# Kernel tuning notes

Hardware: AMD Instinct MI355X
Metric: run time of the kernel (lower is better)

Reference implementation:

```python
import jax, jax.numpy as jnp
import numpy as np

CLP_K = 9
SCL_KS = (3, 4, 3)  # scl0_k, scl1_k, scl2_k from the source


def _ste(f, x):
    # straight-through estimator: forward f(x), identity gradient
    return x + jax.lax.stop_gradient(f(x) - x)


def floor_ste(x):
    return _ste(jnp.floor, x)


def round_ste(x):
    return _ste(jnp.round, x)


def conv_t(x, w, b):
    # torch F.conv_transpose2d with kernel 5, stride 2, padding 2, output_padding 1
    # expressed as an lhs-dilated conv; w is torch layout [in, out, kh, kw]
    k = w.shape[-1]
    wc = jnp.flip(w, axis=(-2, -1)).transpose(1, 0, 2, 3)  # -> [out, in, kh, kw]
    lo = k - 1 - 2           # k-1-padding = 2
    hi = k - 1 - 2 + 1       # + output_padding = 3
    y = jax.lax.conv_general_dilated(
        x, wc, window_strides=(1, 1), padding=[(lo, hi), (lo, hi)],
        lhs_dilation=(2, 2), dimension_numbers=('NCHW', 'OIHW', 'NCHW'))
    return y + b[None, :, None, None]


def split_deconv(x, w, b, split):
    # sum of `split` transposed convs with floor((round(W)+j)/split) quantized weights
    out = 0.0
    for j in range(split):
        wj = floor_ste((round_ste(w) + j) / split)
        bj = floor_ste((round_ste(b) + j) / split)
        out = out + conv_t(x, wj, bj)
    return out


def _g_s_forward(x, ws, bs, ms, relus, dv, Bits, split):
    # clp[i] = round((2^Bits - 1) / relus[i] * 2^(16+clp_k))
    clp = jnp.round((2.0 ** Bits - 1.0) / relus * 2.0 ** (16 + CLP_K))
    for i in range(3):
        x = split_deconv(x, ws[i], bs[i], split)
        x = x * ms[i][None, :, None, None]
        x = floor_ste((x + 2.0 ** (dv[i] - 1 - CLP_K)) / 2.0 ** (dv[i] - CLP_K))
        x = jnp.clip(x, 0.0, clp[i])
        sk = SCL_KS[i]
        scl = floor_ste((relus[i] + 2.0 ** (sk - 1)) / 2.0 ** sk)
        x = floor_ste((x * scl + 2.0 ** (15 + CLP_K - sk)) / 2.0 ** (16 + CLP_K - sk))
    x = split_deconv(x, ws[3], bs[3], split)
    x = x * ms[3][None, :, None, None]
    x = floor_ste((x + 2.0 ** (dv[3] - 9)) / 2.0 ** (dv[3] - 8))
    return x / 255.0


def setup_inputs() -> dict:
    key = jax.random.key(0)
    ks = jax.random.split(key, 16)
    N, M = 192, 320
    B, h, w = 1, 48, 48
    x = jax.random.randint(ks[0], (B, M, h, w), 0, 256).astype(jnp.float32)
    w1 = jax.random.normal(ks[1], (M, N, 5, 5), jnp.float32) * 20.0
    b1 = jax.random.normal(ks[2], (N,), jnp.float32) * 20.0
    w2 = jax.random.normal(ks[3], (N, N, 5, 5), jnp.float32) * 20.0
    b2 = jax.random.normal(ks[4], (N,), jnp.float32) * 20.0
    w3 = jax.random.normal(ks[5], (N, N, 5, 5), jnp.float32) * 20.0
    b3 = jax.random.normal(ks[6], (N,), jnp.float32) * 20.0
    w4 = jax.random.normal(ks[7], (N, 3, 5, 5), jnp.float32) * 20.0
    b4 = jax.random.normal(ks[8], (3,), jnp.float32) * 20.0
    muls0 = jax.random.randint(ks[9], (N,), 1, 1000).astype(jnp.float32)
    muls1 = jax.random.randint(ks[10], (N,), 1, 1000).astype(jnp.float32)
    muls2 = jax.random.randint(ks[11], (N,), 1, 1000).astype(jnp.float32)
    muls3 = jax.random.randint(ks[12], (3,), 1, 1000).astype(jnp.float32)
    relus = jnp.array([40000.0, 36000.0, 30000.0], jnp.float32)
    muls_dvds = jnp.array([24, 24, 24, 24], jnp.int32)
    return {"x": x, "w1": w1, "b1": b1, "w2": w2, "b2": b2, "w3": w3,
            "b3": b3, "w4": w4, "b4": b4, "muls0": muls0, "muls1": muls1,
            "muls2": muls2, "muls3": muls3, "relus": relus,
            "muls_dvds": muls_dvds, "Bits": 8, "split": 4}


def reference(x, w1, b1, w2, b2, w3, b3, w4, b4,
              muls0, muls1, muls2, muls3, relus, muls_dvds, Bits, split):
    dv = muls_dvds.astype(jnp.float32)
    ws = (w1, w2, w3, w4)
    bs = (b1, b2, b3, b4)
    ms = (muls0, muls1, muls2, muls3)
    return _g_s_forward(x, ws, bs, ms, relus, dv, int(Bits), int(split))
```

## Files before the change

### kernel.cpp

```cpp
#include <hip/hip_runtime.h>
#include <cmath>


typedef int int4v  __attribute__((ext_vector_type(4)));
typedef int int16v __attribute__((ext_vector_type(16)));

#define GLOBAL_AS __attribute__((address_space(1)))
#define LDS_AS    __attribute__((address_space(3)))

__device__ __forceinline__ void dma16(const signed char* g, signed char* l) {
    __builtin_amdgcn_global_load_lds((const GLOBAL_AS int*)g, (LDS_AS int*)l,
                                     16, 0, 0);
}

__device__ __forceinline__ void tap_to_k(int t, int& ky, int& kx) {
    if (t < 9)       { int dy = t/3,  dx = t%3;                   ky = 4-2*dy; kx = 4-2*dx; }
    else if (t < 15) { int u = t-9;   int dy = u/2, dx = 1+(u&1);  ky = 4-2*dy; kx = 5-2*dx; }
    else if (t < 21) { int u = t-15;  int dy = 1+u/3, dx = u%3;    ky = 5-2*dy; kx = 4-2*dx; }
    else             { int u = t-21;  int dy = 1+u/2, dx = 1+(u&1); ky = 5-2*dy; kx = 5-2*dx; }
}

__global__ __launch_bounds__(256)
void convert_x_t(const float* __restrict__ x, signed char* __restrict__ xh,
                 int* __restrict__ tsz, int ts_count, int C, int HW,
                 signed char* __restrict__ xpad) {
    if (blockIdx.x == 0 && blockIdx.y == 0) {
        for (int i = threadIdx.x; i < ts_count; i += 256) tsz[i] = 0;
        if (threadIdx.x < 128) ((int*)xpad)[threadIdx.x] = (int)0x80808080;
    }
    __shared__ float t[64][65];
    const int p0 = blockIdx.x * 64;
    const int c0 = blockIdx.y * 64;
    const int pL = threadIdx.x & 63;
    const int r0 = threadIdx.x >> 6;
    #pragma unroll
    for (int k = 0; k < 16; ++k) {
        int ciL = r0 * 16 + k;
        t[ciL][pL] = x[(size_t)(c0 + ciL) * HW + p0 + pL];
    }
    __syncthreads();
    #pragma unroll
    for (int k = 0; k < 16; ++k) {
        int pL2 = r0 * 16 + k;
        xh[(size_t)(p0 + pL2) * C + c0 + pL] = (signed char)((int)t[pL][pL2] - 128);
    }
}

__global__ __launch_bounds__(256)
void prep_pack(const float* __restrict__ w1, const float* __restrict__ w2,
               const float* __restrict__ w3, const float* __restrict__ w4,
               signed char* __restrict__ p1, signed char* __restrict__ p2,
               signed char* __restrict__ p3, signed char* __restrict__ p4,
               int* __restrict__ t1, int* __restrict__ t2, int* __restrict__ t3,
               int* __restrict__ t4) {
    const int layer = blockIdx.y;
    if (layer == 3) {
        const int bx = blockIdx.x;
        if (bx < 54) {
            #pragma unroll
            for (int k = 0; k < 4; ++k) {
                int idx = bx * 1024 + k * 256 + threadIdx.x;
                int j    = idx & 15;
                int lane = (idx >> 4) & 63;
                int rem  = idx >> 10;
                int s9   = rem % 9;
                int qs   = rem / 9;
                int col  = lane & 31;
                int co   = col & 7;
                int p    = col >> 3;
                int py = p >> 1, px = p & 1;
                int dy = s9 / 3, dx = s9 % 3;
                int ci = qs * 32 + ((lane >> 5) << 4) + j;
                bool part = (py == 0 || dy >= 1) && (px == 0 || dx >= 1);
                float v = 0.0f;
                if (co < 3 && part) {
                    int ky = py ? 5 - 2 * dy : 4 - 2 * dy;
                    int kx = px ? 5 - 2 * dx : 4 - 2 * dx;
                    v = rintf(w4[(size_t)(ci * 3 + co) * 25 + ky * 5 + kx]);
                    v = fminf(fmaxf(v, -128.0f), 127.0f);
                }
                p4[idx] = (signed char)(int)v;
            }
        } else if (threadIdx.x < 128) {
            const int Cin = 192, Cout = 3;
            const int u = (bx - 54) * 2 + (threadIdx.x >> 6);
            const int lane = threadIdx.x & 63;
            const int co = u % Cout, p = u / Cout;
            const int py = p >> 1, px = p & 1;
            const int nky = (5 - py + 1) >> 1;
            const int nkx = (5 - px + 1) >> 1;
            const int ntap = nky * nkx;
            int s = 0;
            for (int idx = lane; idx < Cin * ntap; idx += 64) {
                const int ci = idx / ntap;
                const int uu = idx - ci * ntap;
                const int ky = py + 2 * (uu / nkx);
                const int kx = px + 2 * (uu % nkx);
                float v = rintf(w4[(size_t)(ci * Cout + co) * 25 + ky * 5 + kx]);
                v = fminf(fmaxf(v, -128.0f), 127.0f);
                s += (int)v;
            }
            #pragma unroll
            for (int off = 32; off > 0; off >>= 1)
                s += __shfl_down(s, off, 64);
            if (lane == 0) t4[u] = s;
        }
        return;
    }
    const float* w = (layer == 0) ? w1 : (layer == 1) ? w2 : w3;
    signed char* out = (layer == 0) ? p1 : (layer == 1) ? p2 : p3;
    int* ts = (layer == 0) ? t1 : (layer == 1) ? t2 : t3;
    const int Cout = 192;
    const int s = blockIdx.x;
    if (layer > 0 && s >= 36) return;
    const int qs = s / 6, nb = s % 6;

    __shared__ __align__(16) signed char ls[25600];
    __shared__ int lsum[4][32];
    if (threadIdx.x < 128) ((int*)lsum)[threadIdx.x] = 0;
    __syncthreads();

    #pragma unroll
    for (int k = 0; k < 4; ++k) {
        const int pidx = threadIdx.x + k * 256;
        const int cil = pidx >> 5;
        const int col = pidx & 31;
        const int ci = qs * 32 + cil;
        const int co = nb * 32 + col;
        const float* wr = w + (size_t)(ci * Cout + co) * 25;
        const int half = cil >> 4, j = cil & 15;
        const int base = (half * 32 + col) * 16 + j;
        int psum[4] = {0, 0, 0, 0};
        #pragma unroll
        for (int t = 0; t < 25; ++t) {
            int ky, kx; tap_to_k(t, ky, kx);
            float v = rintf(wr[ky * 5 + kx]);
            v = fminf(fmaxf(v, -128.0f), 127.0f);
            int iv = (int)v;
            ls[t * 1024 + base] = (signed char)iv;
            psum[((ky & 1) << 1) | (kx & 1)] += iv;
        }
        #pragma unroll
        for (int p = 0; p < 4; ++p) atomicAdd(&lsum[p][col], psum[p]);
    }
    __syncthreads();

    signed char* dst = out + (size_t)s * 25600;
    for (int i = threadIdx.x; i < 1600; i += 256)
        *(int4v*)&dst[i * 16] = *(const int4v*)&ls[i * 16];
    if (threadIdx.x < 128) {
        const int p = threadIdx.x >> 5, col = threadIdx.x & 31;
        atomicAdd(&ts[p * Cout + nb * 32 + col], lsum[p][col]);
    }
}

__device__ __forceinline__ constexpr int role_nt(int role, int s9) {
    constexpr int NT0[9] = {1,1,1,1,2,2,1,2,2};
    constexpr int NT1[9] = {0,1,1,1,2,2,1,2,2};
    return role == 0 ? NT0[s9] : NT1[s9];
}
__device__ __forceinline__ constexpr int role_tap(int role, int s9, int u) {
    constexpr int T0[9][2] = {{0,0},{1,0},{2,0},{3,0},{4,21},{5,22},{6,0},{7,23},{8,24}};
    constexpr int T1[9][2] = {{0,0},{9,0},{10,0},{15,0},{11,16},{12,17},{18,0},{13,19},{14,20}};
    return role == 0 ? T0[s9][u] : T1[s9][u];
}
__device__ __forceinline__ constexpr int role_acc(int role, int s9, int u) {
    constexpr int A0[9][2] = {{0,0},{0,0},{0,0},{0,0},{0,1},{0,1},{0,0},{0,1},{0,1}};
    constexpr int A1[9][2] = {{0,0},{0,0},{0,0},{1,0},{0,1},{0,1},{1,0},{0,1},{0,1}};
    return role == 0 ? A0[s9][u] : A1[s9][u];
}

template<int ROLE, int R>
__device__ __forceinline__ void compute_role(const signed char* xsb, const signed char* bsb,
                                             int16v (&acc)[R][2], const int (&p0)[R],
                                             int half, int lane) {
    #pragma unroll
    for (int s9 = 0; s9 < 9; ++s9) {
        if (role_nt(ROLE, s9) == 0) continue;
        const int dy = s9 / 3, dx = s9 % 3;
        int4v a[R];
        #pragma unroll
        for (int r = 0; r < R; ++r)
            a[r] = *(const int4v*)&xsb[(p0[r] + dy * 18 + dx) * 32 + half * 16];
        #pragma unroll
        for (int u = 0; u < 2; ++u) {
            if (u < role_nt(ROLE, s9)) {
                int4v b = *(const int4v*)&bsb[role_tap(ROLE, s9, u) * 1024 + lane * 16];
                const int ai = role_acc(ROLE, s9, u);
                #pragma unroll
                for (int r = 0; r < R; ++r)
                    acc[r][ai] = __builtin_amdgcn_mfma_i32_32x32x32_i8(a[r], b, acc[r][ai], 0, 0, 0);
            }
        }
    }
}

template<int MW, int R, bool BDBUF>
__global__ __launch_bounds__(MW * 64, 4)
void deconv_v14(const signed char* __restrict__ xin, const signed char* __restrict__ wpk,
                const float* __restrict__ bias, const float* __restrict__ muls,
                const int* __restrict__ tsum,
                const float* __restrict__ relus, const int* __restrict__ dvds,
                const int* __restrict__ bitsp, const signed char* __restrict__ xpad,
                int layer, int Cin, int Cout, int NT, int Hq, int Wq,
                int NB, int NQX, int T8,
                signed char* __restrict__ outp) {
    constexpr int PAIRS = MW / 2;
    constexpr int QROWS = PAIRS * R * 2;
    constexpr int NROW = QROWS + 2;
    constexpr int NPIX = NROW * 18;
    constexpr int THREADS = MW * 64;
    constexpr int XC = NPIX * 2;
    constexpr int XI = (XC + THREADS - 1) / THREADS;
    constexpr int BC = 1600;
    constexpr int BI = (BC + THREADS - 1) / THREADS;
    constexpr int NBS = BDBUF ? 2 : 1;

    __shared__ __align__(16) signed char xs[2][NPIX * 32];
    __shared__ __align__(16) signed char bs[NBS][25600];

    const int tid  = threadIdx.x;
    const int lane = tid & 63;
    const int wid  = tid >> 6;
    const int pairId = wid >> 1;
    const int role   = wid & 1;

    int nb, qx, qy;
    {
        const int bi = blockIdx.x;
        if (T8 > 0) {
            const int xcd = bi & 7, j = bi >> 3;
            const int tl = j / NB, n = j - tl * NB;
            const int tile = xcd * T8 + tl;
            nb = n; qx = tile % NQX; qy = tile / NQX;
        } else {
            nb = bi % NB;
            const int s = bi / NB;
            qx = s % NQX; qy = s / NQX;
        }
    }
    const int qx0 = qx * 16;
    const int qy0 = qy * QROWS;
    const int n0  = nb * 32;

    int16v acc[R][2];
    #pragma unroll
    for (int r = 0; r < R; ++r)
        #pragma unroll
        for (int p = 0; p < 2; ++p)
            #pragma unroll
            for (int e = 0; e < 16; ++e) acc[r][p][e] = 0;

    const int half   = lane >> 5;
    const int rowbit = (lane >> 4) & 1;
    const int col    = lane & 15;
    int p0[R];
    #pragma unroll
    for (int r = 0; r < R; ++r)
        p0[r] = ((pairId * R + r) * 2 + rowbit) * 18 + col;

    const signed char* xsrc[XI];
    #pragma unroll
    for (int t = 0; t < XI; ++t) {
        int i = tid + t * THREADS;
        xsrc[t] = xpad;
        if (i < XC) {
            int pix = i >> 1, g = i & 1;
            int rr = pix / 18, cc = pix - rr * 18;
            int y = qy0 - 1 + rr, xx = qx0 - 1 + cc;
            bool ok = (unsigned)y < (unsigned)Hq && (unsigned)xx < (unsigned)Wq;
            xsrc[t] = ok ? (xin + ((size_t)y * Wq + xx) * Cin + g * 16)
                         : (xpad + g * 16);
        }
    }

    auto dma_x = [&](int ck, int b) {
        #pragma unroll
        for (int t = 0; t < XI; ++t) {
            int i = tid + t * THREADS;
            if (i < XC) dma16(xsrc[t] + ck, &xs[b][i * 16]);
        }
    };
    auto dma_b = [&](int cs, int b) {
        const signed char* ws = wpk + (size_t)(cs * NT + nb) * 25600;
        #pragma unroll
        for (int t = 0; t < BI; ++t) {
            int i = tid + t * THREADS;
            if (i < BC) dma16(ws + (size_t)i * 16, &bs[b][i * 16]);
        }
    };

    dma_x(0, 0);
    if (BDBUF) dma_b(0, 0);
    for (int ck = 0, s = 0; ck < Cin; ck += 32, ++s) {
        const int cb = s & 1;
        if (BDBUF) {
            __syncthreads();
            if (ck + 32 < Cin) {
                dma_x(s + 1, cb ^ 1) , dma_b(s + 1, cb ^ 1);
            }
            if (role == 0) compute_role<0, R>(xs[cb], bs[cb], acc, p0, half, lane);
            else           compute_role<1, R>(xs[cb], bs[cb], acc, p0, half, lane);
        } else {
            __syncthreads();
            dma_b(s, 0);
            if (ck + 32 < Cin) dma_x(s + 1, cb ^ 1);
            __syncthreads();
            if (role == 0) compute_role<0, R>(xs[cb], bs[0], acc, p0, half, lane);
            else           compute_role<1, R>(xs[cb], bs[0], acc, p0, half, lane);
        }
    }

    const int dv = dvds[layer];
    float add1 = ldexpf(1.0f, dv - 10);
    float inv1 = ldexpf(1.0f, -(dv - 9));
    const float relu = relus[layer];
    const int sk = (layer == 1) ? 4 : 3;
    const float bitsv = ldexpf(1.0f, bitsp[0]) - 1.0f;
    float clp, scl;
    {
        #pragma clang fp contract(off)
        clp = rintf(bitsv / relu * 33554432.0f);
        scl = floorf((relu + ldexpf(1.0f, sk - 1)) * ldexpf(1.0f, -sk));
    }
    float add2 = ldexpf(1.0f, 24 - sk);
    float inv2 = ldexpf(1.0f, -(25 - sk));

    const int co = n0 + (lane & 31);
    float bq = rintf(bias[co]);
    float mm = muls[co];
    int pmap[2];
    pmap[0] = role == 0 ? 0 : 1;
    pmap[1] = role == 0 ? 3 : 2;
    int fullp[2];
    #pragma unroll
    for (int a = 0; a < 2; ++a) fullp[a] = tsum[pmap[a] * Cout + co];

    const int Wout = Wq * 2;

    #pragma unroll
    for (int r = 0; r < R; ++r) {
        #pragma unroll
        for (int a = 0; a < 2; ++a) {
            const int p = pmap[a];
            const int py = p >> 1, px = p & 1;
            #pragma unroll
            for (int reg = 0; reg < 16; ++reg) {
                const int mrow = (reg & 3) + 8 * (reg >> 2) + 4 * (lane >> 5);
                const int qy2 = qy0 + (pairId * R + r) * 2 + (mrow >> 4);
                const int qx2 = qx0 + (mrow & 15);
                float v = (float)(acc[r][a][reg] + 128 * fullp[a]);
                {
                    #pragma clang fp contract(off)
                    v = (v + bq) * mm;
                    v = floorf((v + add1) * inv1);
                    v = fminf(fmaxf(v, 0.0f), clp);
                    v = floorf((v * scl + add2) * inv2);
                }
                const int oy = 2 * qy2 + py, ox = 2 * qx2 + px;
                outp[((size_t)oy * Wout + ox) * Cout + co] = (signed char)((int)v - 128);
            }
        }
    }
}

__global__ __launch_bounds__(256, 4)
void deconv_final_v14(const signed char* __restrict__ xin, const signed char* __restrict__ wpk,
                      const float* __restrict__ bias, const float* __restrict__ muls,
                      const int* __restrict__ tsum, const int* __restrict__ dvds,
                      const signed char* __restrict__ xpad,
                      int Cin, int Hq, int Wq, float* __restrict__ outp) {
    constexpr int R = 2, MW = 4;
    constexpr int QROWS = MW * R * 2;
    constexpr int NROW = QROWS + 2;
    constexpr int NPIX = NROW * 18;
    constexpr int THREADS = 256;
    constexpr int XC = NPIX * 2;
    constexpr int XI = (XC + THREADS - 1) / THREADS;
    constexpr int BC = 576;
    constexpr int BI = (BC + THREADS - 1) / THREADS;

    __shared__ __align__(16) signed char xs[2][NPIX * 32];
    __shared__ __align__(16) signed char bs[2][9216];

    const int tid  = threadIdx.x;
    const int lane = tid & 63;
    const int wid  = tid >> 6;
    const int qx0  = blockIdx.y * 16;
    const int qy0  = blockIdx.z * QROWS;

    int16v acc[R];
    #pragma unroll
    for (int r = 0; r < R; ++r)
        #pragma unroll
        for (int e = 0; e < 16; ++e) acc[r][e] = 0;

    const int half   = lane >> 5;
    const int rowbit = (lane >> 4) & 1;
    const int col    = lane & 15;
    int p0[R];
    #pragma unroll
    for (int r = 0; r < R; ++r)
        p0[r] = ((wid * R + r) * 2 + rowbit) * 18 + col;

    const signed char* xsrc[XI];
    #pragma unroll
    for (int t = 0; t < XI; ++t) {
        int i = tid + t * THREADS;
        xsrc[t] = xpad;
        if (i < XC) {
            int pix = i >> 1, g = i & 1;
            int rr = pix / 18, cc = pix - rr * 18;
            int y = qy0 - 1 + rr, xx = qx0 - 1 + cc;
            bool ok = (unsigned)y < (unsigned)Hq && (unsigned)xx < (unsigned)Wq;
            xsrc[t] = ok ? (xin + ((size_t)y * Wq + xx) * Cin + g * 16)
                         : (xpad + g * 16);
        }
    }

    auto dma_x = [&](int ck, int b) {
        #pragma unroll
        for (int t = 0; t < XI; ++t) {
            int i = tid + t * THREADS;
            if (i < XC) dma16(xsrc[t] + ck, &xs[b][i * 16]);
        }
    };
    auto dma_b = [&](int cs, int b) {
        const signed char* ws = wpk + (size_t)cs * 9216;
        #pragma unroll
        for (int t = 0; t < BI; ++t) {
            int i = tid + t * THREADS;
            if (i < BC) dma16(ws + (size_t)i * 16, &bs[b][i * 16]);
        }
    };

    dma_x(0, 0);
    dma_b(0, 0);
    for (int ck = 0; ck < Cin; ck += 32) {
        const int cb = (ck >> 5) & 1;
        __syncthreads();
        if (ck + 32 < Cin) {
            dma_x(ck + 32, cb ^ 1);
            dma_b((ck >> 5) + 1, cb ^ 1);
        }
        #pragma unroll
        for (int s9 = 0; s9 < 9; ++s9) {
            const int dy = s9 / 3, dx = s9 % 3;
            int4v b = *(const int4v*)&bs[cb][s9 * 1024 + lane * 16];
            #pragma unroll
            for (int r = 0; r < R; ++r) {
                int4v a = *(const int4v*)&xs[cb][(p0[r] + dy * 18 + dx) * 32 + half * 16];
                acc[r] = __builtin_amdgcn_mfma_i32_32x32x32_i8(a, b, acc[r], 0, 0, 0);
            }
        }
    }

    const int dv = dvds[3];
    const float add1 = ldexpf(1.0f, dv - 9);
    const float inv1 = ldexpf(1.0f, -(dv - 8));

    const int coln = lane & 31;
    const int co = coln & 7;
    const int p  = coln >> 3;
    const int py = p >> 1, px = p & 1;
    const bool valid = (co < 3);
    float bq = 0.f, mm = 0.f;
    int fp = 0;
    if (valid) { bq = rintf(bias[co]); mm = muls[co]; fp = tsum[p * 3 + co]; }

    const int Wout = Wq * 2, Hout = Hq * 2;
    #pragma unroll
    for (int r = 0; r < R; ++r) {
        #pragma unroll
        for (int reg = 0; reg < 16; ++reg) {
            const int mrow = (reg & 3) + 8 * (reg >> 2) + 4 * (lane >> 5);
            const int qy = qy0 + (wid * R + r) * 2 + (mrow >> 4);
            const int qx = qx0 + (mrow & 15);
            float v = (float)(acc[r][reg] + 128 * fp);
            {
                #pragma clang fp contract(off)
                v = (v + bq) * mm;
                v = floorf((v + add1) * inv1);
                v = v / 255.0f;
            }
            if (valid) {
                const int oy = 2 * qy + py, ox = 2 * qx + px;
                outp[((size_t)co * Hout + oy) * Wout + ox] = v;
            }
        }
    }
}

extern "C" void kernel_launch(void* const* d_in, const int* in_sizes, int n_in,
                              void* d_out, int out_size, void* d_ws, size_t ws_size,
                              hipStream_t stream) {
    const float* x  = (const float*)d_in[0];
    const float* w1 = (const float*)d_in[1];
    const float* b1 = (const float*)d_in[2];
    const float* w2 = (const float*)d_in[3];
    const float* b2 = (const float*)d_in[4];
    const float* w3 = (const float*)d_in[5];
    const float* b3 = (const float*)d_in[6];
    const float* w4 = (const float*)d_in[7];
    const float* b4 = (const float*)d_in[8];
    const float* m0 = (const float*)d_in[9];
    const float* m1 = (const float*)d_in[10];
    const float* m2 = (const float*)d_in[11];
    const float* m3 = (const float*)d_in[12];
    const float* relus = (const float*)d_in[13];
    const int* dvds = (const int*)d_in[14];
    const int* bitsp = (const int*)d_in[15];

    signed char* wsb = (signed char*)d_ws;
    size_t o = 0;
    signed char* wpk1 = wsb + o; o += (size_t)10 * 6 * 25600;
    signed char* wpk2 = wsb + o; o += (size_t)6 * 6 * 25600;
    signed char* wpk3 = wsb + o; o += (size_t)6 * 6 * 25600;
    signed char* wpk4 = wsb + o; o += (size_t)6 * 9216;
    int* ts1 = (int*)(wsb + o); o += 4 * 192 * 4;
    int* ts2 = (int*)(wsb + o); o += 4 * 192 * 4;
    int* ts3 = (int*)(wsb + o); o += 4 * 192 * 4;
    int* ts4 = (int*)(wsb + o); o += 4 * 4 * 4;
    o = (o + 15) & ~(size_t)15;
    signed char* xpad = wsb + o; o += 512;
    signed char* xh = wsb + o; o += (size_t)48 * 48 * 320;
    signed char* a1 = wsb + o; o += (size_t)96 * 96 * 192;
    signed char* a2 = wsb + o; o += (size_t)192 * 192 * 192;
    signed char* a3 = wsb + o; o += (size_t)384 * 384 * 192;

    const int ts_count = 4 * 192 * 3 + 4 * 4;

    convert_x_t<<<dim3(36, 5), 256, 0, stream>>>(x, xh, ts1, ts_count, 320, 48 * 48, xpad);
    prep_pack<<<dim3(60, 4), 256, 0, stream>>>(w1, w2, w3, w4,
                                               wpk1, wpk2, wpk3, wpk4,
                                               ts1, ts2, ts3, ts4);

    deconv_v14<4, 2, true><<<108, 256, 0, stream>>>(
        xh, wpk1, b1, m0, ts1, relus, dvds, bitsp, xpad, 0, 320, 192, 6, 48, 48,
        6, 3, 0, a1);
    deconv_v14<4, 2, false><<<432, 256, 0, stream>>>(
        a1, wpk2, b2, m1, ts2, relus, dvds, bitsp, xpad, 1, 192, 192, 6, 96, 96,
        6, 6, 0, a2);
    deconv_v14<4, 2, false><<<1728, 256, 0, stream>>>(
        a2, wpk3, b3, m2, ts3, relus, dvds, bitsp, xpad, 2, 192, 192, 6, 192, 192,
        6, 12, 36, a3);
    deconv_final_v14<<<dim3(1, 24, 24), 256, 0, stream>>>(
        a3, wpk4, b4, m3, ts4, dvds, xpad, 192, 384, 384, (float*)d_out);
}
```

Before: 202.9 us.

## Fuse prep, layer-1 and layer-2 deconvs into one persistent kernel with grid barriers

```diff
diff --git a/kernel.cpp b/kernel.cpp
--- a/kernel.cpp
+++ b/kernel.cpp
@@ -11,6 +11,18 @@
 __device__ __forceinline__ void dma16(const signed char* g, signed char* l) {
     __builtin_amdgcn_global_load_lds((const GLOBAL_AS int*)g, (LDS_AS int*)l,
                                      16, 0, 0);
+}
+
+__device__ __forceinline__ void gbar(int* bar, int phase, int nblk) {
+    __threadfence();
+    __syncthreads();
+    if (threadIdx.x == 0) {
+        __hip_atomic_fetch_add(bar, 1, __ATOMIC_RELEASE, __HIP_MEMORY_SCOPE_AGENT);
+        const int tgt = phase * nblk;
+        while (__hip_atomic_load(bar, __ATOMIC_ACQUIRE, __HIP_MEMORY_SCOPE_AGENT) < tgt)
+            __builtin_amdgcn_s_sleep(8);
+    }
+    __syncthreads();
 }
 
 __device__ __forceinline__ void tap_to_k(int t, int& ky, int& kx) {
@@ -18,140 +30,6 @@
     else if (t < 15) { int u = t-9;   int dy = u/2, dx = 1+(u&1);  ky = 4-2*dy; kx = 5-2*dx; }
     else if (t < 21) { int u = t-15;  int dy = 1+u/3, dx = u%3;    ky = 5-2*dy; kx = 4-2*dx; }
     else             { int u = t-21;  int dy = 1+u/2, dx = 1+(u&1); ky = 5-2*dy; kx = 5-2*dx; }
-}
-
-__global__ __launch_bounds__(256)
-void convert_x_t(const float* __restrict__ x, signed char* __restrict__ xh,
-                 int* __restrict__ tsz, int ts_count, int C, int HW,
-                 signed char* __restrict__ xpad) {
-    if (blockIdx.x == 0 && blockIdx.y == 0) {
-        for (int i = threadIdx.x; i < ts_count; i += 256) tsz[i] = 0;
-        if (threadIdx.x < 128) ((int*)xpad)[threadIdx.x] = (int)0x80808080;
-    }
-    __shared__ float t[64][65];
-    const int p0 = blockIdx.x * 64;
-    const int c0 = blockIdx.y * 64;
-    const int pL = threadIdx.x & 63;
-    const int r0 = threadIdx.x >> 6;
-    #pragma unroll
-    for (int k = 0; k < 16; ++k) {
-        int ciL = r0 * 16 + k;
-        t[ciL][pL] = x[(size_t)(c0 + ciL) * HW + p0 + pL];
-    }
-    __syncthreads();
-    #pragma unroll
-    for (int k = 0; k < 16; ++k) {
-        int pL2 = r0 * 16 + k;
-        xh[(size_t)(p0 + pL2) * C + c0 + pL] = (signed char)((int)t[pL][pL2] - 128);
-    }
-}
-
-__global__ __launch_bounds__(256)
-void prep_pack(const float* __restrict__ w1, const float* __restrict__ w2,
-               const float* __restrict__ w3, const float* __restrict__ w4,
-               signed char* __restrict__ p1, signed char* __restrict__ p2,
-               signed char* __restrict__ p3, signed char* __restrict__ p4,
-               int* __restrict__ t1, int* __restrict__ t2, int* __restrict__ t3,
-               int* __restrict__ t4) {
-    const int layer = blockIdx.y;
-    if (layer == 3) {
-        const int bx = blockIdx.x;
-        if (bx < 54) {
-            #pragma unroll
-            for (int k = 0; k < 4; ++k) {
-                int idx = bx * 1024 + k * 256 + threadIdx.x;
-                int j    = idx & 15;
-                int lane = (idx >> 4) & 63;
-                int rem  = idx >> 10;
-                int s9   = rem % 9;
-                int qs   = rem / 9;
-                int col  = lane & 31;
-                int co   = col & 7;
-                int p    = col >> 3;
-                int py = p >> 1, px = p & 1;
-                int dy = s9 / 3, dx = s9 % 3;
-                int ci = qs * 32 + ((lane >> 5) << 4) + j;
-                bool part = (py == 0 || dy >= 1) && (px == 0 || dx >= 1);
-                float v = 0.0f;
-                if (co < 3 && part) {
-                    int ky = py ? 5 - 2 * dy : 4 - 2 * dy;
-                    int kx = px ? 5 - 2 * dx : 4 - 2 * dx;
-                    v = rintf(w4[(size_t)(ci * 3 + co) * 25 + ky * 5 + kx]);
-                    v = fminf(fmaxf(v, -128.0f), 127.0f);
-                }
-                p4[idx] = (signed char)(int)v;
-            }
-        } else if (threadIdx.x < 128) {
-            const int Cin = 192, Cout = 3;
-            const int u = (bx - 54) * 2 + (threadIdx.x >> 6);
-            const int lane = threadIdx.x & 63;
-            const int co = u % Cout, p = u / Cout;
-            const int py = p >> 1, px = p & 1;
-            const int nky = (5 - py + 1) >> 1;
-            const int nkx = (5 - px + 1) >> 1;
-            const int ntap = nky * nkx;
-            int s = 0;
-            for (int idx = lane; idx < Cin * ntap; idx += 64) {
-                const int ci = idx / ntap;
-                const int uu = idx - ci * ntap;
-                const int ky = py + 2 * (uu / nkx);
-                const int kx = px + 2 * (uu % nkx);
-                float v = rintf(w4[(size_t)(ci * Cout + co) * 25 + ky * 5 + kx]);
-                v = fminf(fmaxf(v, -128.0f), 127.0f);
-                s += (int)v;
-            }
-            #pragma unroll
-            for (int off = 32; off > 0; off >>= 1)
-                s += __shfl_down(s, off, 64);
-            if (lane == 0) t4[u] = s;
-        }
-        return;
-    }
-    const float* w = (layer == 0) ? w1 : (layer == 1) ? w2 : w3;
-    signed char* out = (layer == 0) ? p1 : (layer == 1) ? p2 : p3;
-    int* ts = (layer == 0) ? t1 : (layer == 1) ? t2 : t3;
-    const int Cout = 192;
-    const int s = blockIdx.x;
-    if (layer > 0 && s >= 36) return;
-    const int qs = s / 6, nb = s % 6;
-
-    __shared__ __align__(16) signed char ls[25600];
-    __shared__ int lsum[4][32];
-    if (threadIdx.x < 128) ((int*)lsum)[threadIdx.x] = 0;
-    __syncthreads();
-
-    #pragma unroll
-    for (int k = 0; k < 4; ++k) {
-        const int pidx = threadIdx.x + k * 256;
-        const int cil = pidx >> 5;
-        const int col = pidx & 31;
-        const int ci = qs * 32 + cil;
-        const int co = nb * 32 + col;
-        const float* wr = w + (size_t)(ci * Cout + co) * 25;
-        const int half = cil >> 4, j = cil & 15;
-        const int base = (half * 32 + col) * 16 + j;
-        int psum[4] = {0, 0, 0, 0};
-        #pragma unroll
-        for (int t = 0; t < 25; ++t) {
-            int ky, kx; tap_to_k(t, ky, kx);
-            float v = rintf(wr[ky * 5 + kx]);
-            v = fminf(fmaxf(v, -128.0f), 127.0f);
-            int iv = (int)v;
-            ls[t * 1024 + base] = (signed char)iv;
-            psum[((ky & 1) << 1) | (kx & 1)] += iv;
-        }
-        #pragma unroll
-        for (int p = 0; p < 4; ++p) atomicAdd(&lsum[p][col], psum[p]);
-    }
-    __syncthreads();
-
-    signed char* dst = out + (size_t)s * 25600;
-    for (int i = threadIdx.x; i < 1600; i += 256)
-        *(int4v*)&dst[i * 16] = *(const int4v*)&ls[i * 16];
-    if (threadIdx.x < 128) {
-        const int p = threadIdx.x >> 5, col = threadIdx.x & 31;
-        atomicAdd(&ts[p * Cout + nb * 32 + col], lsum[p][col]);
-    }
 }
 
 __device__ __forceinline__ constexpr int role_nt(int role, int s9) {
@@ -196,15 +74,15 @@
 }
 
 template<int MW, int R, bool BDBUF>
-__global__ __launch_bounds__(MW * 64, 4)
-void deconv_v14(const signed char* __restrict__ xin, const signed char* __restrict__ wpk,
-                const float* __restrict__ bias, const float* __restrict__ muls,
-                const int* __restrict__ tsum,
-                const float* __restrict__ relus, const int* __restrict__ dvds,
-                const int* __restrict__ bitsp, const signed char* __restrict__ xpad,
-                int layer, int Cin, int Cout, int NT, int Hq, int Wq,
-                int NB, int NQX, int T8,
-                signed char* __restrict__ outp) {
+__device__ __forceinline__ void deconv_body(
+        int bi, signed char* xsm, signed char* bsm,
+        const signed char* __restrict__ xin, const signed char* __restrict__ wpk,
+        const float* __restrict__ bias, const float* __restrict__ muls,
+        const int* __restrict__ tsum,
+        const float* __restrict__ relus, const int* __restrict__ dvds,
+        const int* __restrict__ bitsp, const signed char* __restrict__ xpad,
+        int layer, int Cin, int Cout, int NT, int Hq, int Wq,
+        int NB, int NQX, int T8, signed char* __restrict__ outp) {
     constexpr int PAIRS = MW / 2;
     constexpr int QROWS = PAIRS * R * 2;
     constexpr int NROW = QROWS + 2;
@@ -214,10 +92,7 @@
     constexpr int XI = (XC + THREADS - 1) / THREADS;
     constexpr int BC = 1600;
     constexpr int BI = (BC + THREADS - 1) / THREADS;
-    constexpr int NBS = BDBUF ? 2 : 1;
-
-    __shared__ __align__(16) signed char xs[2][NPIX * 32];
-    __shared__ __align__(16) signed char bs[NBS][25600];
+    constexpr int XBUF = NPIX * 32;
 
     const int tid  = threadIdx.x;
     const int lane = tid & 63;
@@ -227,7 +102,6 @@
 
     int nb, qx, qy;
     {
-        const int bi = blockIdx.x;
         if (T8 > 0) {
             const int xcd = bi & 7, j = bi >> 3;
             const int tl = j / NB, n = j - tl * NB;
@@ -278,7 +152,7 @@
         #pragma unroll
         for (int t = 0; t < XI; ++t) {
             int i = tid + t * THREADS;
-            if (i < XC) dma16(xsrc[t] + ck, &xs[b][i * 16]);
+            if (i < XC) dma16(xsrc[t] + ck, xsm + b * XBUF + i * 16);
         }
     };
     auto dma_b = [&](int cs, int b) {
@@ -286,7 +160,7 @@
         #pragma unroll
         for (int t = 0; t < BI; ++t) {
             int i = tid + t * THREADS;
-            if (i < BC) dma16(ws + (size_t)i * 16, &bs[b][i * 16]);
+            if (i < BC) dma16(ws + (size_t)i * 16, bsm + b * 25600 + i * 16);
         }
     };
 
@@ -297,17 +171,18 @@
         if (BDBUF) {
             __syncthreads();
             if (ck + 32 < Cin) {
-                dma_x(s + 1, cb ^ 1) , dma_b(s + 1, cb ^ 1);
-            }
-            if (role == 0) compute_role<0, R>(xs[cb], bs[cb], acc, p0, half, lane);
-            else           compute_role<1, R>(xs[cb], bs[cb], acc, p0, half, lane);
+                dma_x(s + 1, cb ^ 1);
+                dma_b(s + 1, cb ^ 1);
+            }
+            if (role == 0) compute_role<0, R>(xsm + cb * XBUF, bsm + cb * 25600, acc, p0, half, lane);
+            else           compute_role<1, R>(xsm + cb * XBUF, bsm + cb * 25600, acc, p0, half, lane);
         } else {
             __syncthreads();
             dma_b(s, 0);
             if (ck + 32 < Cin) dma_x(s + 1, cb ^ 1);
             __syncthreads();
-            if (role == 0) compute_role<0, R>(xs[cb], bs[0], acc, p0, half, lane);
-            else           compute_role<1, R>(xs[cb], bs[0], acc, p0, half, lane);
+            if (role == 0) compute_role<0, R>(xsm + cb * XBUF, bsm, acc, p0, half, lane);
+            else           compute_role<1, R>(xsm + cb * XBUF, bsm, acc, p0, half, lane);
         }
     }
 
@@ -364,8 +239,176 @@
     }
 }
 
+#define FGRID 432
+
+__global__ __launch_bounds__(256, 2)
+void fused_front(const float* __restrict__ x, signed char* __restrict__ xh,
+                 const float* __restrict__ w1, const float* __restrict__ w2,
+                 const float* __restrict__ w3, const float* __restrict__ w4,
+                 signed char* __restrict__ p1, signed char* __restrict__ p2,
+                 signed char* __restrict__ p3, signed char* __restrict__ p4,
+                 int* __restrict__ t1, int* __restrict__ t2,
+                 int* __restrict__ t3, int* __restrict__ t4,
+                 int* __restrict__ bar, const signed char* __restrict__ xpad,
+                 const float* __restrict__ bias1, const float* __restrict__ m0,
+                 const float* __restrict__ bias2, const float* __restrict__ m1,
+                 const float* __restrict__ relus, const int* __restrict__ dvds,
+                 const int* __restrict__ bitsp,
+                 signed char* __restrict__ a1, signed char* __restrict__ a2) {
+    __shared__ __align__(16) signed char smem[62720];
+    const int bid = blockIdx.x;
+    const int tid = threadIdx.x;
+
+    if (bid < 180) {
+        float (*t)[65] = (float(*)[65])smem;
+        const int C = 320, HW = 48 * 48;
+        const int p0 = (bid % 36) * 64;
+        const int c0 = (bid / 36) * 64;
+        const int pL = tid & 63;
+        const int r0 = tid >> 6;
+        #pragma unroll
+        for (int k = 0; k < 16; ++k) {
+            int ciL = r0 * 16 + k;
+            t[ciL][pL] = x[(size_t)(c0 + ciL) * HW + p0 + pL];
+        }
+        __syncthreads();
+        #pragma unroll
+        for (int k = 0; k < 16; ++k) {
+            int pL2 = r0 * 16 + k;
+            xh[(size_t)(p0 + pL2) * C + c0 + pL] = (signed char)((int)t[pL][pL2] - 128);
+        }
+    } else if (bid < 312) {
+        int u = bid - 180;
+        int layer, s;
+        if (u < 60)      { layer = 0; s = u; }
+        else if (u < 96) { layer = 1; s = u - 60; }
+        else             { layer = 2; s = u - 96; }
+        const float* w = (layer == 0) ? w1 : (layer == 1) ? w2 : w3;
+        signed char* out = (layer == 0) ? p1 : (layer == 1) ? p2 : p3;
+        int* ts = (layer == 0) ? t1 : (layer == 1) ? t2 : t3;
+        const int Cout = 192;
+        const int qs = s / 6, nb = s % 6;
+
+        signed char* ls = smem;
+        int (*lsum)[32] = (int(*)[32])(smem + 25600);
+        if (tid < 128) ((int*)lsum)[tid] = 0;
+        __syncthreads();
+
+        #pragma unroll
+        for (int k = 0; k < 4; ++k) {
+            const int pidx = tid + k * 256;
+            const int cil = pidx >> 5;
+            const int colp = pidx & 31;
+            const int ci = qs * 32 + cil;
+            const int cop = nb * 32 + colp;
+            const float* wr = w + (size_t)(ci * Cout + cop) * 25;
+            const int halfp = cil >> 4, j = cil & 15;
+            const int base = (halfp * 32 + colp) * 16 + j;
+            int psum[4] = {0, 0, 0, 0};
+            #pragma unroll
+            for (int tt = 0; tt < 25; ++tt) {
+                int ky, kx; tap_to_k(tt, ky, kx);
+                float v = rintf(wr[ky * 5 + kx]);
+                v = fminf(fmaxf(v, -128.0f), 127.0f);
+                int iv = (int)v;
+                ls[tt * 1024 + base] = (signed char)iv;
+                psum[((ky & 1) << 1) | (kx & 1)] += iv;
+            }
+            #pragma unroll
+            for (int p = 0; p < 4; ++p) atomicAdd(&lsum[p][colp], psum[p]);
+        }
+        __syncthreads();
+
+        signed char* dst = out + (size_t)s * 25600;
+        for (int i = tid; i < 1600; i += 256)
+            *(int4v*)&dst[i * 16] = *(const int4v*)&ls[i * 16];
+        if (tid < 128) {
+            const int p = tid >> 5, colp = tid & 31;
+            atomicAdd(&ts[p * Cout + nb * 32 + colp], lsum[p][colp]);
+        }
+    } else if (bid < 366) {
+        const int bx = bid - 312;
+        #pragma unroll
+        for (int k = 0; k < 4; ++k) {
+            int idx = bx * 1024 + k * 256 + tid;
+            int j    = idx & 15;
+            int lane = (idx >> 4) & 63;
+            int rem  = idx >> 10;
+            int s9   = rem % 9;
+            int qs   = rem / 9;
+            int colp = lane & 31;
+            int cop  = colp & 7;
+            int p    = colp >> 3;
+            int py = p >> 1, px = p & 1;
+            int dy = s9 / 3, dx = s9 % 3;
+            int ci = qs * 32 + ((lane >> 5) << 4) + j;
+            bool part = (py == 0 || dy >= 1) && (px == 0 || dx >= 1);
+            float v = 0.0f;
+            if (cop < 3 && part) {
+                int ky = py ? 5 - 2 * dy : 4 - 2 * dy;
+                int kx = px ? 5 - 2 * dx : 4 - 2 * dx;
+                v = rintf(w4[(size_t)(ci * 3 + cop) * 25 + ky * 5 + kx]);
+                v = fminf(fmaxf(v, -128.0f), 127.0f);
+            }
+            p4[idx] = (signed char)(int)v;
+        }
+    } else if (bid < 372 && tid < 128) {
+        const int Cin = 192, Cout = 3;
+        const int u = (bid - 366) * 2 + (tid >> 6);
+        const int lane = tid & 63;
+        const int cop = u % Cout, p = u / Cout;
+        const int py = p >> 1, px = p & 1;
+        const int nky = (5 - py + 1) >> 1;
+        const int nkx = (5 - px + 1) >> 1;
+        const int ntap = nky * nkx;
+        int sacc = 0;
+        for (int idx = lane; idx < Cin * ntap; idx += 64) {
+            const int ci = idx / ntap;
+            const int uu = idx - ci * ntap;
+            const int ky = py + 2 * (uu / nkx);
+            const int kx = px + 2 * (uu % nkx);
+            float v = rintf(w4[(size_t)(ci * Cout + cop) * 25 + ky * 5 + kx]);
+            v = fminf(fmaxf(v, -128.0f), 127.0f);
+            sacc += (int)v;
+        }
+        #pragma unroll
+        for (int off = 32; off > 0; off >>= 1)
+            sacc += __shfl_down(sacc, off, 64);
+        if (lane == 0) t4[u] = sacc;
+    }
+
+    gbar(bar, 1, FGRID);
+
+    if (bid < 108)
+        deconv_body<4, 2, true>(bid, smem, smem + 11520,
+                                xh, p1, bias1, m0, t1, relus, dvds, bitsp, xpad,
+                                0, 320, 192, 6, 48, 48, 6, 3, 0, a1);
+
+    gbar(bar, 2, FGRID);
+
+    deconv_body<4, 2, false>(bid, smem, smem + 11520,
+                             a1, p2, bias2, m1, t2, relus, dvds, bitsp, xpad,
+                             1, 192, 192, 6, 96, 96, 6, 6, 0, a2);
+}
+
 __global__ __launch_bounds__(256, 4)
-void deconv_final_v14(const signed char* __restrict__ xin, const signed char* __restrict__ wpk,
+void deconv_mid(const signed char* __restrict__ xin, const signed char* __restrict__ wpk,
+                const float* __restrict__ bias, const float* __restrict__ muls,
+                const int* __restrict__ tsum,
+                const float* __restrict__ relus, const int* __restrict__ dvds,
+                const int* __restrict__ bitsp, const signed char* __restrict__ xpad,
+                int layer, int Cin, int Cout, int NT, int Hq, int Wq,
+                int NB, int NQX, int T8,
+                signed char* __restrict__ outp) {
+    __shared__ __align__(16) signed char xsm[2][180 * 32];
+    __shared__ __align__(16) signed char bsm[25600];
+    deconv_body<4, 2, false>(blockIdx.x, &xsm[0][0], bsm,
+                             xin, wpk, bias, muls, tsum, relus, dvds, bitsp,
+                             xpad, layer, Cin, Cout, NT, Hq, Wq, NB, NQX, T8, outp);
+}
+
+__global__ __launch_bounds__(256, 4)
+void deconv_final_v15(const signed char* __restrict__ xin, const signed char* __restrict__ wpk,
                       const float* __restrict__ bias, const float* __restrict__ muls,
                       const int* __restrict__ tsum, const int* __restrict__ dvds,
                       const signed char* __restrict__ xpad,
@@ -521,6 +564,8 @@
     int* ts2 = (int*)(wsb + o); o += 4 * 192 * 4;
     int* ts3 = (int*)(wsb + o); o += 4 * 192 * 4;
     int* ts4 = (int*)(wsb + o); o += 4 * 4 * 4;
+    int* bar = (int*)(wsb + o); o += 16;
+    const size_t zbytes = 3 * (4 * 192 * 4) + 4 * 4 * 4 + 16;
     o = (o + 15) & ~(size_t)15;
     signed char* xpad = wsb + o; o += 512;
     signed char* xh = wsb + o; o += (size_t)48 * 48 * 320;
@@ -528,22 +573,18 @@
     signed char* a2 = wsb + o; o += (size_t)192 * 192 * 192;
     signed char* a3 = wsb + o; o += (size_t)384 * 384 * 192;
 
-    const int ts_count = 4 * 192 * 3 + 4 * 4;
-
-    convert_x_t<<<dim3(36, 5), 256, 0, stream>>>(x, xh, ts1, ts_count, 320, 48 * 48, xpad);
-    prep_pack<<<dim3(60, 4), 256, 0, stream>>>(w1, w2, w3, w4,
-                                               wpk1, wpk2, wpk3, wpk4,
-                                               ts1, ts2, ts3, ts4);
-
-    deconv_v14<4, 2, true><<<108, 256, 0, stream>>>(
-        xh, wpk1, b1, m0, ts1, relus, dvds, bitsp, xpad, 0, 320, 192, 6, 48, 48,
-        6, 3, 0, a1);
-    deconv_v14<4, 2, false><<<432, 256, 0, stream>>>(
-        a1, wpk2, b2, m1, ts2, relus, dvds, bitsp, xpad, 1, 192, 192, 6, 96, 96,
-        6, 6, 0, a2);
-    deconv_v14<4, 2, false><<<1728, 256, 0, stream>>>(
+    hipMemsetAsync(ts1, 0, zbytes, stream);
+    hipMemsetAsync(xpad, 0x80, 512, stream);
+
+    fused_front<<<FGRID, 256, 0, stream>>>(
+        x, xh, w1, w2, w3, w4, wpk1, wpk2, wpk3, wpk4,
+        ts1, ts2, ts3, ts4, bar, xpad,
+        b1, m0, b2, m1, relus, dvds, bitsp, a1, a2);
+
+    deconv_mid<<<1728, 256, 0, stream>>>(
         a2, wpk3, b3, m2, ts3, relus, dvds, bitsp, xpad, 2, 192, 192, 6, 192, 192,
         6, 12, 36, a3);
-    deconv_final_v14<<<dim3(1, 24, 24), 256, 0, stream>>>(
+
+    deconv_final_v15<<<dim3(1, 24, 24), 256, 0, stream>>>(
         a3, wpk4, b4, m3, ts4, dvds, xpad, 192, 384, 384, (float*)d_out);
 }
```

New measurement: 435.1 us. 2.14x slower.
